# Kernel optimization log

Measured on AMD Instinct MI355X. Metric: run time of the kernel, lower is better.

The kernel has to match this reference:

```python
import jax, jax.numpy as jnp
import numpy as np

B, L, H = 4, 4096, 1024
NH, W, SHIFT, FF = 16, 64, 32, 4096
HD = H // NH
EPS = 1e-5


def _ln(x, g, b):
    mu = jnp.mean(x, axis=-1, keepdims=True)
    var = jnp.var(x, axis=-1, keepdims=True)
    return (x - mu) * jax.lax.rsqrt(var + EPS) * g + b


def setup_inputs() -> dict:
    key = jax.random.key(0)
    ks = jax.random.split(key, 8)
    s = 0.02
    return {
        "x": jax.random.normal(ks[0], (B, L, H), dtype=jnp.float32),
        "ln1_g": jnp.ones((H,), jnp.float32),
        "ln1_b": jnp.zeros((H,), jnp.float32),
        "in_proj_w": jax.random.normal(ks[1], (3 * H, H), jnp.float32) * s,
        "in_proj_b": jnp.zeros((3 * H,), jnp.float32),
        "out_proj_w": jax.random.normal(ks[2], (H, H), jnp.float32) * s,
        "out_proj_b": jnp.zeros((H,), jnp.float32),
        "ln2_g": jnp.ones((H,), jnp.float32),
        "ln2_b": jnp.zeros((H,), jnp.float32),
        "w1": jax.random.normal(ks[3], (FF, H), jnp.float32) * s,
        "b1": jnp.zeros((FF,), jnp.float32),
        "w2": jax.random.normal(ks[4], (H, FF), jnp.float32) * s,
        "b2": jnp.zeros((H,), jnp.float32),
    }


def reference(x, ln1_g, ln1_b, in_proj_w, in_proj_b, out_proj_w, out_proj_b,
              ln2_g, ln2_b, w1, b1, w2, b2):
    # shift (torch.roll with negative shift)
    xs = jnp.roll(x, -SHIFT, axis=1)
    q_in = _ln(xs, ln1_g, ln1_b)
    # packed qkv projection (torch MHA in_proj)
    qkv = q_in @ in_proj_w.T + in_proj_b              # [B, L, 3H]
    q, k, v = jnp.split(qkv, 3, axis=-1)
    nW = L // W
    # block-diagonal mask == independent windows: [B, nW, W, NH, HD]
    def to_win(t):
        return t.reshape(B, nW, W, NH, HD)
    qw, kw, vw = to_win(q), to_win(k), to_win(v)
    scale = 1.0 / jnp.sqrt(jnp.float32(HD))
    scores = jnp.einsum('bnqhd,bnkhd->bnhqk', qw, kw) * scale
    attn = jax.nn.softmax(scores, axis=-1)
    o = jnp.einsum('bnhqk,bnkhd->bnqhd', attn, vw).reshape(B, L, H)
    o = o @ out_proj_w.T + out_proj_b
    xs = xs + o
    x = jnp.roll(xs, SHIFT, axis=1)  # un-shift
    z = _ln(x, ln2_g, ln2_b)
    z = jax.nn.gelu(z @ w1.T + b1, approximate=False) @ w2.T + b2
    return x + z
```

## Files before the change

### kernel.cpp

```cpp
#include <hip/hip_runtime.h>
#include <cstdint>
#include <cstddef>

#define B_ 4
#define L_ 4096
#define H_ 1024
#define NH_ 16
#define W_ 64
#define SHIFT_ 32
#define FF_ 4096
#define HD_ 64
#define MCA_ 8192

typedef unsigned short u16;
typedef __attribute__((ext_vector_type(8))) __bf16 bf16x8;
typedef __attribute__((ext_vector_type(4))) float f32x4;
typedef __attribute__((ext_vector_type(4))) unsigned short u16x4;

__device__ __forceinline__ float bf2f(u16 u) {
    unsigned int x = ((unsigned int)u) << 16;
    float f;
    __builtin_memcpy(&f, &x, 4);
    return f;
}
__device__ __forceinline__ u16 f2bf(float f) {
    unsigned int u;
    __builtin_memcpy(&u, &f, 4);
    u = (u + 0x7fffu + ((u >> 16) & 1u)) >> 16;
    return (u16)u;
}

__device__ __forceinline__ void gload16(const u16* g, u16* l) {
    __builtin_amdgcn_global_load_lds(
        (const __attribute__((address_space(1))) void*)g,
        (__attribute__((address_space(3))) void*)l, 16, 0, 0);
}

__device__ __forceinline__ bf16x8 ldfrag(const u16* p) {
    uint4 v = *(const uint4*)p;
    bf16x8 r;
    __builtin_memcpy(&r, &v, 16);
    return r;
}

__device__ __forceinline__ f32x4 mfma16(bf16x8 a, bf16x8 b, f32x4 c) {
    return __builtin_amdgcn_mfma_f32_16x16x32_bf16(a, b, c, 0, 0, 0);
}

__global__ __launch_bounds__(256) void cvt_kernel(
    const float* __restrict__ src, u16* __restrict__ dst, int n4) {
    const int i = blockIdx.x * 256 + threadIdx.x;
    if (i < n4) {
        const float4 v = ((const float4*)src)[i];
        u16x4 o;
        o[0] = f2bf(v.x); o[1] = f2bf(v.y);
        o[2] = f2bf(v.z); o[3] = f2bf(v.w);
        ((u16x4*)dst)[i] = o;
    }
}

template <int GELU, int BIAS, int F32OUT>
__global__ __launch_bounds__(512, 2) void gemm256(
    const u16* __restrict__ A, const u16* __restrict__ Bm,
    int lda, int ldb, const float* __restrict__ bias,
    void* __restrict__ Cv, int N, int K) {
    __shared__ __align__(16) u16 lds[4 * 16384];

    const int tid = threadIdx.x;
    const int lane = tid & 63;
    const int wv = tid >> 6;
    const int wr = wv >> 2;
    const int wc = wv & 3;
    const int ln15 = lane & 15;
    const int quad = lane >> 4;
    const int mBase = blockIdx.y * 256;
    const int nBase = blockIdx.x * 256;
    const int nt = K >> 5;

    const int sr = tid >> 3;
    const int src = (tid & 7) ^ (sr & 7);
    const int grow = sr * 2 + (src >> 2);
    const int gk = (src & 3) * 8;
    const u16* gA = A + (size_t)(mBase + grow) * lda + gk;
    const u16* gB = Bm + (size_t)(nBase + grow) * ldb + gk;
    u16* dstA = &lds[tid * 8];
    u16* dstB = &lds[8192 + tid * 8];

    const int sw = ((ln15 & 1) * 4 + quad) ^ (ln15 >> 1);
    const int offA = (wr * 64 + (ln15 >> 1)) * 64 + sw * 8;
    const int offB = (wc * 32 + (ln15 >> 1)) * 64 + sw * 8;

    f32x4 acc[8][4] = {};

#pragma unroll
    for (int p = 0; p < 3; ++p) {
        const u16* a = gA + p * 32;
        const u16* b = gB + p * 32;
        u16* la = dstA + p * 16384;
        u16* lb = dstB + p * 16384;
        gload16(a, la);
        gload16(a + (size_t)128 * lda, la + 4096);
        gload16(b, lb);
        gload16(b + (size_t)128 * ldb, lb + 4096);
    }
    asm volatile("s_waitcnt vmcnt(8)" ::: "memory");
    __builtin_amdgcn_s_barrier();
    __builtin_amdgcn_sched_barrier(0);

    for (int tt = 0; tt < nt; ++tt) {
        const u16* lA = &lds[(tt & 3) * 16384];
        const u16* lB = lA + 8192;
        bf16x8 aF[4], bF[4], aG[4];
#pragma unroll
        for (int i = 0; i < 4; ++i) aF[i] = ldfrag(lA + offA + i * 512);
#pragma unroll
        for (int j = 0; j < 4; ++j) bF[j] = ldfrag(lB + offB + j * 512);
        if (tt + 3 < nt) {
            const u16* a = gA + (size_t)(tt + 3) * 32;
            u16* la = dstA + ((tt + 3) & 3) * 16384;
            gload16(a, la);
            gload16(a + (size_t)128 * lda, la + 4096);
        }
        __builtin_amdgcn_s_barrier();
        __builtin_amdgcn_s_setprio(1);
#pragma unroll
        for (int i = 0; i < 4; ++i)
#pragma unroll
            for (int j = 0; j < 4; ++j)
                acc[i][j] = mfma16(aF[i], bF[j], acc[i][j]);
        __builtin_amdgcn_s_setprio(0);
#pragma unroll
        for (int i = 0; i < 4; ++i) aG[i] = ldfrag(lA + offA + (i + 4) * 512);
        if (tt + 3 < nt) {
            const u16* b = gB + (size_t)(tt + 3) * 32;
            u16* lb = dstB + ((tt + 3) & 3) * 16384;
            gload16(b, lb);
            gload16(b + (size_t)128 * ldb, lb + 4096);
        }
        __builtin_amdgcn_s_barrier();
        __builtin_amdgcn_s_setprio(1);
#pragma unroll
        for (int i = 0; i < 4; ++i)
#pragma unroll
            for (int j = 0; j < 4; ++j)
                acc[i + 4][j] = mfma16(aG[i], bF[j], acc[i + 4][j]);
        __builtin_amdgcn_s_setprio(0);
        if (tt < nt - 1) {
            if (tt <= nt - 4)
                asm volatile("s_waitcnt vmcnt(8)" ::: "memory");
            else if (tt == nt - 3)
                asm volatile("s_waitcnt vmcnt(4)" ::: "memory");
            else
                asm volatile("s_waitcnt vmcnt(0)" ::: "memory");
            __builtin_amdgcn_s_barrier();
            __builtin_amdgcn_sched_barrier(0);
        }
    }

    const int r0 = mBase + wr * 128 + quad * 4;
    const int c0 = nBase + wc * 64 + ln15;
#pragma unroll
    for (int fn = 0; fn < 4; ++fn) {
        const int col = c0 + fn * 16;
        const float bcol = BIAS ? bias[col] : 0.0f;
#pragma unroll
        for (int fm = 0; fm < 8; ++fm) {
#pragma unroll
            for (int r = 0; r < 4; ++r) {
                const int row = r0 + fm * 16 + r;
                float v = acc[fm][fn][r] + bcol;
                if (GELU) v = 0.5f * v * (1.0f + erff(v * 0.70710678118f));
                if (F32OUT)
                    ((float*)Cv)[(size_t)row * N + col] += v;
                else
                    ((u16*)Cv)[(size_t)row * N + col] = f2bf(v);
            }
        }
    }
}

__global__ __launch_bounds__(256, 4) void ln1_kernel(
    const float* __restrict__ x, const float* __restrict__ g,
    const float* __restrict__ bb, u16* __restrict__ y, int rowBase) {
    const int row = rowBase + blockIdx.x;
    const int bi = row >> 12, l = row & 4095;
    const float* src = x + ((size_t)(bi << 12) + ((l + SHIFT_) & 4095)) * 1024;
    const int t = threadIdx.x;
    const int lane = t & 63, wv = t >> 6;

    const float4 u = ((const float4*)src)[t];
    float v[4] = {u.x, u.y, u.z, u.w};
    float sum = 0.f, sq = 0.f;
#pragma unroll
    for (int k = 0; k < 4; ++k) { sum += v[k]; sq += v[k] * v[k]; }
    for (int off = 32; off > 0; off >>= 1) {
        sum += __shfl_down(sum, off);
        sq += __shfl_down(sq, off);
    }
    __shared__ float red[8];
    __shared__ float smu, srs;
    if (lane == 0) { red[wv] = sum; red[4 + wv] = sq; }
    __syncthreads();
    if (t == 0) {
        float s = red[0] + red[1] + red[2] + red[3];
        float q = red[4] + red[5] + red[6] + red[7];
        float mu = s * (1.0f / 1024.0f);
        float var = q * (1.0f / 1024.0f) - mu * mu;
        smu = mu;
        srs = rsqrtf(var + 1e-5f);
    }
    __syncthreads();
    const float mu = smu, rs = srs;
    const float4 gv = ((const float4*)g)[t];
    const float4 bv = ((const float4*)bb)[t];
    u16x4 outv;
    outv[0] = f2bf((v[0] - mu) * rs * gv.x + bv.x);
    outv[1] = f2bf((v[1] - mu) * rs * gv.y + bv.y);
    outv[2] = f2bf((v[2] - mu) * rs * gv.z + bv.z);
    outv[3] = f2bf((v[3] - mu) * rs * gv.w + bv.w);
    ((u16x4*)(y + (size_t)blockIdx.x * 1024))[t] = outv;
}

__global__ __launch_bounds__(256, 4) void ln2_kernel(
    const float* __restrict__ x, const u16* __restrict__ o2,
    const float* __restrict__ g, const float* __restrict__ bb,
    float* __restrict__ x2, u16* __restrict__ z) {
    const int row = blockIdx.x;
    const int bi = row >> 12, l = row & 4095;
    const size_t srcO = (size_t)(bi << 12) + ((l - SHIFT_) & 4095);
    const int t = threadIdx.x;
    const int lane = t & 63, wv = t >> 6;

    const float4 ux = ((const float4*)(x + (size_t)row * 1024))[t];
    const u16x4 uo = ((const u16x4*)(o2 + srcO * 1024))[t];
    float v[4];
    v[0] = ux.x + bf2f(uo[0]);
    v[1] = ux.y + bf2f(uo[1]);
    v[2] = ux.z + bf2f(uo[2]);
    v[3] = ux.w + bf2f(uo[3]);
    float sum = 0.f, sq = 0.f;
#pragma unroll
    for (int k = 0; k < 4; ++k) { sum += v[k]; sq += v[k] * v[k]; }
    float4 x2v = {v[0], v[1], v[2], v[3]};
    ((float4*)(x2 + (size_t)row * 1024))[t] = x2v;

    for (int off = 32; off > 0; off >>= 1) {
        sum += __shfl_down(sum, off);
        sq += __shfl_down(sq, off);
    }
    __shared__ float red[8];
    __shared__ float smu, srs;
    if (lane == 0) { red[wv] = sum; red[4 + wv] = sq; }
    __syncthreads();
    if (t == 0) {
        float s = red[0] + red[1] + red[2] + red[3];
        float q = red[4] + red[5] + red[6] + red[7];
        float mu = s * (1.0f / 1024.0f);
        float var = q * (1.0f / 1024.0f) - mu * mu;
        smu = mu;
        srs = rsqrtf(var + 1e-5f);
    }
    __syncthreads();
    const float mu = smu, rs = srs;
    const float4 gv = ((const float4*)g)[t];
    const float4 bv = ((const float4*)bb)[t];
    u16x4 outv;
    outv[0] = f2bf((v[0] - mu) * rs * gv.x + bv.x);
    outv[1] = f2bf((v[1] - mu) * rs * gv.y + bv.y);
    outv[2] = f2bf((v[2] - mu) * rs * gv.z + bv.z);
    outv[3] = f2bf((v[3] - mu) * rs * gv.w + bv.w);
    ((u16x4*)(z + (size_t)row * 1024))[t] = outv;
}

__global__ __launch_bounds__(256, 2) void attn_kernel(
    const u16* __restrict__ qkv, u16* __restrict__ o) {
    __shared__ __align__(16) u16 sQ[64 * 64];
    __shared__ __align__(16) u16 sK[64 * 64];
    __shared__ __align__(16) u16 sV[64 * 64];
    __shared__ float sS[64 * 66];

    const int t = threadIdx.x;
    const int win = blockIdx.x >> 4;
    const int head = blockIdx.x & 15;
    const size_t rowbase = (size_t)win * 64;
    const u16* base = qkv + rowbase * 3072 + head * 64;

    {
        const int c0 = t, c1 = t + 256;
        const int r0 = c0 >> 3, d0 = (c0 & 7) * 8;
        const int r1 = c1 >> 3, d1 = (c1 & 7) * 8;
        const u16* g0 = base + (size_t)r0 * 3072 + d0;
        const u16* g1 = base + (size_t)r1 * 3072 + d1;
        gload16(g0, &sQ[c0 * 8]);
        gload16(g1, &sQ[c1 * 8]);
        gload16(g0 + 1024, &sK[c0 * 8]);
        gload16(g1 + 1024, &sK[c1 * 8]);
        gload16(g0 + 2048, &sV[c0 * 8]);
        gload16(g1 + 2048, &sV[c1 * 8]);
    }
    __syncthreads();

    const int lane = t & 63, wv = t >> 6;
    const int ln15 = lane & 15, quad = lane >> 4;

    f32x4 accS[4] = {};
#pragma unroll
    for (int kb = 0; kb < 2; ++kb) {
        bf16x8 aF = ldfrag(&sQ[(wv * 16 + ln15) * 64 + kb * 32 + quad * 8]);
#pragma unroll
        for (int jt = 0; jt < 4; ++jt) {
            bf16x8 bF = ldfrag(&sK[(jt * 16 + ln15) * 64 + kb * 32 + quad * 8]);
            accS[jt] = mfma16(aF, bF, accS[jt]);
        }
    }
#pragma unroll
    for (int jt = 0; jt < 4; ++jt)
#pragma unroll
        for (int r = 0; r < 4; ++r)
            sS[(wv * 16 + quad * 4 + r) * 66 + jt * 16 + ln15] =
                accS[jt][r] * 0.125f;
    __syncthreads();

    {
        const int row = t >> 2, part = t & 3;
        const float* sr = &sS[row * 66 + part * 16];
        float vals[16];
        float mx = -1e30f;
#pragma unroll
        for (int i = 0; i < 16; ++i) {
            vals[i] = sr[i];
            mx = fmaxf(mx, vals[i]);
        }
        mx = fmaxf(mx, __shfl_xor(mx, 1));
        mx = fmaxf(mx, __shfl_xor(mx, 2));
        float sum = 0.f;
#pragma unroll
        for (int i = 0; i < 16; ++i) {
            vals[i] = __expf(vals[i] - mx);
            sum += vals[i];
        }
        sum += __shfl_xor(sum, 1);
        sum += __shfl_xor(sum, 2);
        const float inv = 1.0f / sum;
        u16* pr = &sQ[row * 64 + part * 16];
#pragma unroll
        for (int i = 0; i < 16; ++i) pr[i] = f2bf(vals[i] * inv);
    }
    __syncthreads();

    f32x4 accO[4] = {};
#pragma unroll
    for (int kb = 0; kb < 2; ++kb) {
        bf16x8 aF = ldfrag(&sQ[(wv * 16 + ln15) * 64 + kb * 32 + quad * 8]);
#pragma unroll
        for (int dt = 0; dt < 4; ++dt) {
            u16 tmp[8];
#pragma unroll
            for (int j = 0; j < 8; ++j)
                tmp[j] = sV[(kb * 32 + quad * 8 + j) * 64 + dt * 16 + ln15];
            bf16x8 bF;
            __builtin_memcpy(&bF, tmp, 16);
            accO[dt] = mfma16(aF, bF, accO[dt]);
        }
    }
    u16* ob = o + rowbase * 1024 + head * 64;
#pragma unroll
    for (int dt = 0; dt < 4; ++dt)
#pragma unroll
        for (int r = 0; r < 4; ++r) {
            const int q = wv * 16 + quad * 4 + r;
            const int d = dt * 16 + ln15;
            ob[(size_t)q * 1024 + d] = f2bf(accO[dt][r]);
        }
}

extern "C" void kernel_launch(void* const* d_in, const int* in_sizes, int n_in,
                              void* d_out, int out_size, void* d_ws,
                              size_t ws_size, hipStream_t stream) {
    (void)in_sizes; (void)n_in; (void)out_size; (void)ws_size;
    const float* x = (const float*)d_in[0];
    const float* ln1_g = (const float*)d_in[1];
    const float* ln1_b = (const float*)d_in[2];
    const float* in_proj_w = (const float*)d_in[3];
    const float* in_proj_b = (const float*)d_in[4];
    const float* out_proj_w = (const float*)d_in[5];
    const float* out_proj_b = (const float*)d_in[6];
    const float* ln2_g = (const float*)d_in[7];
    const float* ln2_b = (const float*)d_in[8];
    const float* w1 = (const float*)d_in[9];
    const float* b1 = (const float*)d_in[10];
    const float* w2 = (const float*)d_in[11];
    const float* b2 = (const float*)d_in[12];
    float* out = (float*)d_out;

    char* ws = (char*)d_ws;
    const size_t MB = 1024 * 1024;
    u16* wb_w1 = (u16*)(ws + 0 * MB);
    u16* wb_w2 = (u16*)(ws + 8 * MB);
    u16* wb_inproj = (u16*)(ws + 16 * MB);
    u16* wb_outproj = (u16*)(ws + 22 * MB);
    u16* qkv_c = (u16*)(ws + 24 * MB);
    u16* o2 = (u16*)(ws + 72 * MB);
    u16* z = (u16*)(ws + 16 * MB);
    u16* h_buf = (u16*)(ws + 48 * MB);

    u16* qin = (u16*)d_out;
    u16* o_full = (u16*)((char*)d_out + 16 * MB);
    float* x2 = out;

    const int M = B_ * L_;

    cvt_kernel<<<(FF_ * H_ / 4 + 255) / 256, 256, 0, stream>>>(
        w1, wb_w1, FF_ * H_ / 4);
    cvt_kernel<<<(H_ * FF_ / 4 + 255) / 256, 256, 0, stream>>>(
        w2, wb_w2, H_ * FF_ / 4);
    cvt_kernel<<<(3 * H_ * H_ / 4 + 255) / 256, 256, 0, stream>>>(
        in_proj_w, wb_inproj, 3 * H_ * H_ / 4);
    cvt_kernel<<<(H_ * H_ / 4 + 255) / 256, 256, 0, stream>>>(
        out_proj_w, wb_outproj, H_ * H_ / 4);

    for (int c = 0; c < 2; ++c) {
        const int rowBase = c * MCA_;
        ln1_kernel<<<MCA_, 256, 0, stream>>>(x, ln1_g, ln1_b, qin, rowBase);
        gemm256<0, 1, 0><<<dim3(3 * H_ / 256, MCA_ / 256), 512, 0, stream>>>(
            qin, wb_inproj, H_, H_, in_proj_b, qkv_c, 3 * H_, H_);
        attn_kernel<<<(MCA_ / W_) * NH_, 256, 0, stream>>>(
            qkv_c, o_full + (size_t)rowBase * H_);
    }
    gemm256<0, 1, 0><<<dim3(H_ / 256, M / 256), 512, 0, stream>>>(
        o_full, wb_outproj, H_, H_, out_proj_b, o2, H_, H_);

    ln2_kernel<<<M, 256, 0, stream>>>(x, o2, ln2_g, ln2_b, x2, z);

    gemm256<1, 1, 0><<<dim3(2048 / 256, M / 256), 512, 0, stream>>>(
        z, wb_w1, H_, H_, b1, h_buf, 2048, H_);
    gemm256<0, 0, 1><<<dim3(H_ / 256, M / 256), 512, 0, stream>>>(
        h_buf, wb_w2, 2048, FF_, nullptr, out, H_, 2048);
    gemm256<1, 1, 0><<<dim3(2048 / 256, M / 256), 512, 0, stream>>>(
        z, wb_w1 + (size_t)2048 * H_, H_, H_, b1 + 2048, h_buf, 2048, H_);
    gemm256<0, 1, 1><<<dim3(H_ / 256, M / 256), 512, 0, stream>>>(
        h_buf, wb_w2 + 2048, 2048, FF_, b2, out, H_, 2048);
}
```

Baseline: 908.4 us.

## Restructure GEMM to double-buffered K=64 tiles with LDS-staged coalesced epilogue

Rewrites the 256x256 GEMM main loop from a 4-stage K=32 ring buffer into a double-buffered K=64 scheme, using a different LDS swizzle and fewer barriers per K step. For bf16 outputs, results are staged through LDS and written out as 16-byte coalesced stores instead of scattered 2-byte stores. The two-chunk LN1/QKV/attention loop becomes a single full-size launch, with workspace offsets moved to make room. The trade-off is less prefetch depth, which may expose more global-load latency, plus an extra LDS round trip and barrier in the epilogue.

```diff
diff --git a/kernel.cpp b/kernel.cpp
--- a/kernel.cpp
+++ b/kernel.cpp
@@ -10,7 +10,6 @@
 #define SHIFT_ 32
 #define FF_ 4096
 #define HD_ 64
-#define MCA_ 8192
 
 typedef unsigned short u16;
 typedef __attribute__((ext_vector_type(8))) __bf16 bf16x8;
@@ -64,7 +63,10 @@
     const u16* __restrict__ A, const u16* __restrict__ Bm,
     int lda, int ldb, const float* __restrict__ bias,
     void* __restrict__ Cv, int N, int K) {
-    __shared__ __align__(16) u16 lds[4 * 16384];
+    __shared__ __align__(16) u16 sA0[16384];
+    __shared__ __align__(16) u16 sA1[16384];
+    __shared__ __align__(16) u16 sB0[16384];
+    __shared__ __align__(16) u16 sB1[16384];
 
     const int tid = threadIdx.x;
     const int lane = tid & 63;
@@ -75,114 +77,122 @@
     const int quad = lane >> 4;
     const int mBase = blockIdx.y * 256;
     const int nBase = blockIdx.x * 256;
-    const int nt = K >> 5;
-
-    const int sr = tid >> 3;
-    const int src = (tid & 7) ^ (sr & 7);
-    const int grow = sr * 2 + (src >> 2);
-    const int gk = (src & 3) * 8;
-    const u16* gA = A + (size_t)(mBase + grow) * lda + gk;
-    const u16* gB = Bm + (size_t)(nBase + grow) * ldb + gk;
-    u16* dstA = &lds[tid * 8];
-    u16* dstB = &lds[8192 + tid * 8];
-
-    const int sw = ((ln15 & 1) * 4 + quad) ^ (ln15 >> 1);
-    const int offA = (wr * 64 + (ln15 >> 1)) * 64 + sw * 8;
-    const int offB = (wc * 32 + (ln15 >> 1)) * 64 + sw * 8;
+    const int nt = K >> 6;
+
+    const int srow = tid >> 3;
+    const int sk = ((tid & 7) ^ (srow & 7)) * 8;
+    const u16* gA = A + (size_t)(mBase + srow) * lda + sk;
+    const u16* gB = Bm + (size_t)(nBase + srow) * ldb + sk;
+    const size_t ldas = (size_t)lda * 64;
+    const size_t ldbs = (size_t)ldb * 64;
+
+    const int rbA = (wr * 128 + ln15) * 64;
+    const int rbB = (wc * 64 + ln15) * 64;
+    const int sw0 = (quad ^ (ln15 & 7)) * 8;
+    const int sw1 = ((4 + quad) ^ (ln15 & 7)) * 8;
 
     f32x4 acc[8][4] = {};
 
-#pragma unroll
-    for (int p = 0; p < 3; ++p) {
-        const u16* a = gA + p * 32;
-        const u16* b = gB + p * 32;
-        u16* la = dstA + p * 16384;
-        u16* lb = dstB + p * 16384;
-        gload16(a, la);
-        gload16(a + (size_t)128 * lda, la + 4096);
-        gload16(b, lb);
-        gload16(b + (size_t)128 * ldb, lb + 4096);
-    }
-    asm volatile("s_waitcnt vmcnt(8)" ::: "memory");
-    __builtin_amdgcn_s_barrier();
-    __builtin_amdgcn_sched_barrier(0);
-
-    for (int tt = 0; tt < nt; ++tt) {
-        const u16* lA = &lds[(tt & 3) * 16384];
-        const u16* lB = lA + 8192;
-        bf16x8 aF[4], bF[4], aG[4];
-#pragma unroll
-        for (int i = 0; i < 4; ++i) aF[i] = ldfrag(lA + offA + i * 512);
-#pragma unroll
-        for (int j = 0; j < 4; ++j) bF[j] = ldfrag(lB + offB + j * 512);
-        if (tt + 3 < nt) {
-            const u16* a = gA + (size_t)(tt + 3) * 32;
-            u16* la = dstA + ((tt + 3) & 3) * 16384;
-            gload16(a, la);
-            gload16(a + (size_t)128 * lda, la + 4096);
-        }
-        __builtin_amdgcn_s_barrier();
-        __builtin_amdgcn_s_setprio(1);
-#pragma unroll
-        for (int i = 0; i < 4; ++i)
-#pragma unroll
-            for (int j = 0; j < 4; ++j)
-                acc[i][j] = mfma16(aF[i], bF[j], acc[i][j]);
-        __builtin_amdgcn_s_setprio(0);
-#pragma unroll
-        for (int i = 0; i < 4; ++i) aG[i] = ldfrag(lA + offA + (i + 4) * 512);
-        if (tt + 3 < nt) {
-            const u16* b = gB + (size_t)(tt + 3) * 32;
-            u16* lb = dstB + ((tt + 3) & 3) * 16384;
-            gload16(b, lb);
-            gload16(b + (size_t)128 * ldb, lb + 4096);
-        }
-        __builtin_amdgcn_s_barrier();
-        __builtin_amdgcn_s_setprio(1);
-#pragma unroll
-        for (int i = 0; i < 4; ++i)
-#pragma unroll
-            for (int j = 0; j < 4; ++j)
-                acc[i + 4][j] = mfma16(aG[i], bF[j], acc[i + 4][j]);
-        __builtin_amdgcn_s_setprio(0);
-        if (tt < nt - 1) {
-            if (tt <= nt - 4)
-                asm volatile("s_waitcnt vmcnt(8)" ::: "memory");
-            else if (tt == nt - 3)
-                asm volatile("s_waitcnt vmcnt(4)" ::: "memory");
-            else
-                asm volatile("s_waitcnt vmcnt(0)" ::: "memory");
-            __builtin_amdgcn_s_barrier();
-            __builtin_amdgcn_sched_barrier(0);
-        }
-    }
-
-    const int r0 = mBase + wr * 128 + quad * 4;
-    const int c0 = nBase + wc * 64 + ln15;
-#pragma unroll
-    for (int fn = 0; fn < 4; ++fn) {
-        const int col = c0 + fn * 16;
-        const float bcol = BIAS ? bias[col] : 0.0f;
-#pragma unroll
-        for (int fm = 0; fm < 8; ++fm) {
-#pragma unroll
-            for (int r = 0; r < 4; ++r) {
-                const int row = r0 + fm * 16 + r;
-                float v = acc[fm][fn][r] + bcol;
-                if (GELU) v = 0.5f * v * (1.0f + erff(v * 0.70710678118f));
-                if (F32OUT)
-                    ((float*)Cv)[(size_t)row * N + col] += v;
-                else
-                    ((u16*)Cv)[(size_t)row * N + col] = f2bf(v);
+#define STAGE_T(g, ld64, buf)                          \
+    do {                                               \
+        const u16* _g = (g);                           \
+        gload16(_g, (buf) + tid * 8);                  \
+        gload16(_g + (ld64), (buf) + 4096 + tid * 8);  \
+        gload16(_g + 2 * (ld64), (buf) + 8192 + tid * 8);  \
+        gload16(_g + 3 * (ld64), (buf) + 12288 + tid * 8); \
+    } while (0)
+
+#define HALF(CA, CB, SW)                                             \
+    do {                                                             \
+        bf16x8 a_[8], b_[4];                                         \
+        _Pragma("unroll") for (int fm = 0; fm < 8; ++fm)             \
+            a_[fm] = ldfrag((CA) + rbA + fm * 1024 + (SW));          \
+        _Pragma("unroll") for (int fn = 0; fn < 4; ++fn)             \
+            b_[fn] = ldfrag((CB) + rbB + fn * 1024 + (SW));          \
+        __builtin_amdgcn_s_setprio(1);                               \
+        _Pragma("unroll") for (int fm = 0; fm < 8; ++fm)             \
+            _Pragma("unroll") for (int fn = 0; fn < 4; ++fn)         \
+                acc[fm][fn] = mfma16(a_[fm], b_[fn], acc[fm][fn]);   \
+        __builtin_amdgcn_s_setprio(0);                               \
+    } while (0)
+
+#define TILE(CA, CB, PA, PB, tn)                            \
+    do {                                                    \
+        const bool _st = (tn) < nt;                         \
+        if (_st) STAGE_T(gA + (size_t)(tn) * 64, ldas, PA); \
+        HALF(CA, CB, sw0);                                  \
+        if (_st) STAGE_T(gB + (size_t)(tn) * 64, ldbs, PB); \
+        HALF(CA, CB, sw1);                                  \
+        __syncthreads();                                    \
+    } while (0)
+
+    STAGE_T(gA, ldas, sA0);
+    STAGE_T(gB, ldbs, sB0);
+    __syncthreads();
+
+    for (int t = 0; t < nt; t += 2) {
+        TILE(sA0, sB0, sA1, sB1, t + 1);
+        TILE(sA1, sB1, sA0, sB0, t + 2);
+    }
+
+    if (F32OUT) {
+        float* C = (float*)Cv;
+        const int r0 = mBase + wr * 128 + quad * 4;
+        const int c0 = nBase + wc * 64 + ln15;
+#pragma unroll
+        for (int fn = 0; fn < 4; ++fn) {
+            const int col = c0 + fn * 16;
+            const float bcol = BIAS ? bias[col] : 0.0f;
+#pragma unroll
+            for (int fm = 0; fm < 8; ++fm) {
+#pragma unroll
+                for (int r = 0; r < 4; ++r) {
+                    const int row = r0 + fm * 16 + r;
+                    float v = acc[fm][fn][r] + bcol;
+                    if (GELU) v = 0.5f * v * (1.0f + erff(v * 0.70710678118f));
+                    C[(size_t)row * N + col] += v;
+                }
             }
         }
-    }
+    } else {
+        u16* lo = wr ? sB0 : sA0;
+        u16* hi = wr ? sB1 : sA1;
+#pragma unroll
+        for (int fn = 0; fn < 4; ++fn) {
+            const int col = wc * 64 + fn * 16 + ln15;
+            const float bcol = BIAS ? bias[nBase + col] : 0.0f;
+#pragma unroll
+            for (int fm = 0; fm < 8; ++fm) {
+                u16* wb = (fm < 4) ? lo : hi;
+#pragma unroll
+                for (int r = 0; r < 4; ++r) {
+                    float v = acc[fm][fn][r] + bcol;
+                    if (GELU) v = 0.5f * v * (1.0f + erff(v * 0.70710678118f));
+                    wb[((fm & 3) * 16 + quad * 4 + r) * 256 + col] = f2bf(v);
+                }
+            }
+        }
+        __syncthreads();
+        u16* Cu = (u16*)Cv;
+        const int rr = tid >> 5;
+        const int cc = (tid & 31) * 8;
+#pragma unroll
+        for (int p = 0; p < 16; ++p) {
+            const u16* rb = (p < 4) ? sA0 : (p < 8) ? sA1 : (p < 12) ? sB0 : sB1;
+            const uint4 vv =
+                *(const uint4*)(rb + ((p & 3) * 16 + rr) * 256 + cc);
+            *(uint4*)(Cu + (size_t)(mBase + p * 16 + rr) * N + nBase + cc) = vv;
+        }
+    }
+#undef TILE
+#undef HALF
+#undef STAGE_T
 }
 
 __global__ __launch_bounds__(256, 4) void ln1_kernel(
     const float* __restrict__ x, const float* __restrict__ g,
-    const float* __restrict__ bb, u16* __restrict__ y, int rowBase) {
-    const int row = rowBase + blockIdx.x;
+    const float* __restrict__ bb, u16* __restrict__ y) {
+    const int row = blockIdx.x;
     const int bi = row >> 12, l = row & 4095;
     const float* src = x + ((size_t)(bi << 12) + ((l + SHIFT_) & 4095)) * 1024;
     const int t = threadIdx.x;
@@ -218,7 +228,7 @@
     outv[1] = f2bf((v[1] - mu) * rs * gv.y + bv.y);
     outv[2] = f2bf((v[2] - mu) * rs * gv.z + bv.z);
     outv[3] = f2bf((v[3] - mu) * rs * gv.w + bv.w);
-    ((u16x4*)(y + (size_t)blockIdx.x * 1024))[t] = outv;
+    ((u16x4*)(y + (size_t)row * 1024))[t] = outv;
 }
 
 __global__ __launch_bounds__(256, 4) void ln2_kernel(
@@ -399,13 +409,13 @@
     u16* wb_w2 = (u16*)(ws + 8 * MB);
     u16* wb_inproj = (u16*)(ws + 16 * MB);
     u16* wb_outproj = (u16*)(ws + 22 * MB);
-    u16* qkv_c = (u16*)(ws + 24 * MB);
-    u16* o2 = (u16*)(ws + 72 * MB);
+    u16* qkv = (u16*)(ws + 24 * MB);
+    u16* o2 = (u16*)(ws + 88 * MB);
     u16* z = (u16*)(ws + 16 * MB);
     u16* h_buf = (u16*)(ws + 48 * MB);
 
     u16* qin = (u16*)d_out;
-    u16* o_full = (u16*)((char*)d_out + 16 * MB);
+    u16* o_full = (u16*)((char*)d_out + 32 * MB);
     float* x2 = out;
 
     const int M = B_ * L_;
@@ -419,14 +429,10 @@
     cvt_kernel<<<(H_ * H_ / 4 + 255) / 256, 256, 0, stream>>>(
         out_proj_w, wb_outproj, H_ * H_ / 4);
 
-    for (int c = 0; c < 2; ++c) {
-        const int rowBase = c * MCA_;
-        ln1_kernel<<<MCA_, 256, 0, stream>>>(x, ln1_g, ln1_b, qin, rowBase);
-        gemm256<0, 1, 0><<<dim3(3 * H_ / 256, MCA_ / 256), 512, 0, stream>>>(
-            qin, wb_inproj, H_, H_, in_proj_b, qkv_c, 3 * H_, H_);
-        attn_kernel<<<(MCA_ / W_) * NH_, 256, 0, stream>>>(
-            qkv_c, o_full + (size_t)rowBase * H_);
-    }
+    ln1_kernel<<<M, 256, 0, stream>>>(x, ln1_g, ln1_b, qin);
+    gemm256<0, 1, 0><<<dim3(3 * H_ / 256, M / 256), 512, 0, stream>>>(
+        qin, wb_inproj, H_, H_, in_proj_b, qkv, 3 * H_, H_);
+    attn_kernel<<<(M / W_) * NH_, 256, 0, stream>>>(qkv, o_full);
     gemm256<0, 1, 0><<<dim3(H_ / 256, M / 256), 512, 0, stream>>>(
         o_full, wb_outproj, H_, H_, out_proj_b, o2, H_, H_);
 
```

New measurement: 851.0 us. 6.3% less time.
